# Performance work log

Hardware: AMD Instinct MI355X
Metric: run time of the kernel (lower is better)

The kernel has to match this reference:

```python
import jax, jax.numpy as jnp
import numpy as np

EPS = 1e-12  # F.normalize default eps (denominator = max(norm, eps))


def setup_inputs() -> dict:
    key = jax.random.key(0)
    ks = jax.random.split(key, 8)
    B, FIN, H, W = 4, 256, 64, 64
    N_MEM, SQ = 64, 16           # sqrt_fin = fin**0.5
    POS_CH = 2                    # PosEncoding concatenates one coord channel per dim
    CIN = FIN + POS_CH
    QK = N_MEM * SQ               # 1024
    # PosEncoding buffer: normalized coordinate grid in [-1, 1], shape [2, H, W]
    ys = jnp.linspace(-1.0, 1.0, H, dtype=jnp.float32)
    xs = jnp.linspace(-1.0, 1.0, W, dtype=jnp.float32)
    gy, gx = jnp.meshgrid(ys, xs, indexing='ij')
    pos = jnp.stack([gy, gx], axis=0)
    s = 0.02
    return {
        'x':    jax.random.normal(ks[0], (B, FIN, H, W), jnp.float32),
        'pos':  pos,
        'wq':   jax.random.normal(ks[1], (QK, CIN), jnp.float32) * s,
        'bq':   jnp.zeros((QK,), jnp.float32),
        'wk':   jax.random.normal(ks[2], (QK, CIN), jnp.float32) * s,
        'bk':   jnp.zeros((QK,), jnp.float32),
        'v':    jax.random.normal(ks[3], (N_MEM, FIN), jnp.float32) * s,
        'wout': jax.random.normal(ks[4], (FIN, FIN), jnp.float32) * s,
        'bout': jnp.zeros((FIN,), jnp.float32),
    }


def reference(x, pos, wq, bq, wk, bk, v, wout, bout):
    B, C, H, W = x.shape
    S = H * W
    n_mem, fin = v.shape
    sq = wq.shape[0] // n_mem
    # PosEncoding: concat coordinate channels
    posb = jnp.broadcast_to(pos[None], (B,) + pos.shape)
    xp = jnp.concatenate([x, posb], axis=1).reshape(B, C + pos.shape[0], S)
    # 1x1 conv projections (channel GEMMs)
    q = jnp.einsum('oc,bcs->bos', wq, xp) + bq[None, :, None]  # [B, n_mem*sq, S]
    k = jnp.einsum('oc,bcs->bos', wk, xp) + bk[None, :, None]
    q = q.reshape(B, n_mem, sq, S).transpose(0, 3, 1, 2)  # [B,S,m,sq]
    k = k.reshape(B, n_mem, sq, S).transpose(0, 3, 2, 1)  # [B,S,sq,m]
    # F.normalize: q over last dim (sqrt_fin), k over dim=1 (sqrt_fin)
    qn = q / jnp.maximum(jnp.linalg.norm(q, axis=-1, keepdims=True), EPS)
    kn = k / jnp.maximum(jnp.linalg.norm(k, axis=2, keepdims=True), EPS)
    # attn[b,s,m,n] = qn . kn ; dropout is identity in eval mode.
    # mean over memory slots m commutes with (attn @ v), so fuse:
    attn_mean = jnp.einsum('bsk,bskn->bsn', qn.mean(axis=2), kn)  # [B,S,n_mem]
    mem = attn_mean @ v                                            # [B,S,fin]
    mem = mem.transpose(0, 2, 1).reshape(B, fin, H, W)
    out = jnp.einsum('of,bfhw->bohw', wout, mem) + bout[None, :, None, None]
    return x + out
```

## Files before the change

### kernel.cpp

```cpp
#include <hip/hip_runtime.h>
#include <stdint.h>

#define EPSN 1e-12f

typedef float f32x16 __attribute__((ext_vector_type(16)));
typedef float f32x4 __attribute__((ext_vector_type(4)));
typedef __bf16 bf16x8 __attribute__((ext_vector_type(8)));

__device__ __forceinline__ unsigned short f2bf(float f) {
  union { float f; unsigned int u; } v; v.f = f;
  unsigned int u = v.u + 0x7FFFu + ((v.u >> 16) & 1u);
  return (unsigned short)(u >> 16);
}

#define WQF_OFF 0
#define WKF_OFF (32 * 18 * 64 * 8)
#define WVP_OFF (2 * 32 * 18 * 64 * 8)

__global__ __launch_bounds__(256) void prep_kernel(
    const float* __restrict__ wq, const float* __restrict__ bq,
    const float* __restrict__ wk, const float* __restrict__ bk,
    const float* __restrict__ v, const float* __restrict__ wout,
    unsigned short* __restrict__ wsp) {
  int bid = blockIdx.x;
  if (bid < 512) {
    int isK = bid >= 256;
    int ob = (bid & 255) * 4;
    const float* w = isK ? wk : wq;
    const float* bb = isK ? bk : bq;
    unsigned short* dst = wsp + (isK ? WKF_OFF : WQF_OFF);
    for (int i = threadIdx.x; i < 4 * 129; i += 256) {
      int r = i / 129, q = i - r * 129;
      int o = ob + r, k = q * 2;
      float2 w2 = *(const float2*)(w + o * 258 + k);
      int g = o >> 5, col = o & 31;
      int ks = k >> 4, hi = (k >> 3) & 1, j = k & 7;
      uint32_t pk = (uint32_t)f2bf(w2.x) | ((uint32_t)f2bf(w2.y) << 16);
      *(uint32_t*)(dst + (((g * 18 + ks) * 64 + hi * 32 + col) << 3) + j) = pk;
    }
    for (int i = threadIdx.x; i < 4 * 30; i += 256) {
      int r = i / 30, kk = 258 + (i - r * 30);
      int o = ob + r;
      int g = o >> 5, col = o & 31;
      int ks = kk >> 4, hi = (kk >> 3) & 1, j = kk & 7;
      dst[(((g * 18 + ks) * 64 + hi * 32 + col) << 3) + j] =
          (kk == 258) ? f2bf(bb[o]) : (unsigned short)0;
    }
  } else {
    int idx = (bid - 512) * 256 + threadIdx.x;
    int fc = idx & 15, m = (idx >> 4) & 63, o = idx >> 10;
    const f32x4* wo = (const f32x4*)(wout + o * 256 + fc * 16);
    const f32x4* vm = (const f32x4*)(v + m * 256 + fc * 16);
    float s = 0.f;
#pragma unroll
    for (int f = 0; f < 4; ++f) {
      f32x4 a = wo[f], bvv = vm[f];
      s += a[0]*bvv[0] + a[1]*bvv[1] + a[2]*bvv[2] + a[3]*bvv[3];
    }
    s += __shfl_xor(s, 1, 64);
    s += __shfl_xor(s, 2, 64);
    s += __shfl_xor(s, 4, 64);
    s += __shfl_xor(s, 8, 64);
    if (fc == 0) wsp[WVP_OFF + o * 64 + m] = f2bf(s);
  }
}

#define QSS 33
#define AT 72

__global__ __launch_bounds__(1024, 4) void fused_kernel(
    const float* __restrict__ x, const float* __restrict__ pos,
    const unsigned short* __restrict__ wsp, const float* __restrict__ bout,
    float* __restrict__ out) {
  __shared__ __align__(16) unsigned short xpF[18 * 2 * 32 * 8];
  __shared__ __align__(16) float qbarL[16 * QSS];
  __shared__ __align__(16) unsigned short attnM[32 * AT];
  __shared__ float boutL[256];

  const int tid = threadIdx.x;
  const int lane = tid & 63;
  const int wid = __builtin_amdgcn_readfirstlane(tid >> 6);
  const int px = lane & 31, q2 = lane >> 5;
  const int P0 = blockIdx.x * 32;
  const int b = P0 >> 12, s0 = P0 & 4095;

  uint32_t* xp32 = (uint32_t*)xpF;
  for (int i = tid; i < 32 * 144; i += 1024) {
    int p = i & 31, dcol = i >> 5;
    int c0 = dcol * 2;
    float v0, v1;
    if (c0 < 256) {
      v0 = x[(b * 256 + c0) * 4096 + s0 + p];
      v1 = x[(b * 256 + c0 + 1) * 4096 + s0 + p];
    } else if (c0 == 256) {
      v0 = pos[s0 + p];
      v1 = pos[4096 + s0 + p];
    } else {
      v0 = (c0 == 258) ? 1.0f : 0.0f;
      v1 = 0.0f;
    }
    xp32[(dcol >> 2) * 128 + p * 4 + (dcol & 3)] =
        (uint32_t)f2bf(v0) | ((uint32_t)f2bf(v1) << 16);
  }
  if (tid < 256) boutL[tid] = bout[tid];
  if (tid < 16 * QSS) qbarL[tid] = 0.f;
  __syncthreads();

  const unsigned short* aq = wsp + WQF_OFF + (2 * wid) * 18 * 512 + lane * 8;
  const unsigned short* ak = wsp + WKF_OFF + (2 * wid) * 18 * 512 + lane * 8;

  f32x16 accq0 = (f32x16)0.f, accq1 = (f32x16)0.f,
         acck0 = (f32x16)0.f, acck1 = (f32x16)0.f;
#pragma unroll 3
  for (int ks = 0; ks < 18; ++ks) {
    bf16x8 bv = *(const bf16x8*)&xpF[(ks * 2 + q2) * 256 + px * 8];
    bf16x8 aq0 = *(const bf16x8*)(aq + ks * 512);
    bf16x8 aq1 = *(const bf16x8*)(aq + 9216 + ks * 512);
    bf16x8 ak0 = *(const bf16x8*)(ak + ks * 512);
    bf16x8 ak1 = *(const bf16x8*)(ak + 9216 + ks * 512);
    accq0 = __builtin_amdgcn_mfma_f32_32x32x16_bf16(aq0, bv, accq0, 0, 0, 0);
    accq1 = __builtin_amdgcn_mfma_f32_32x32x16_bf16(aq1, bv, accq1, 0, 0, 0);
    acck0 = __builtin_amdgcn_mfma_f32_32x32x16_bf16(ak0, bv, acck0, 0, 0, 0);
    acck1 = __builtin_amdgcn_mfma_f32_32x32x16_bf16(ak1, bv, acck1, 0, 0, 0);
  }

  {
    float qsum[8];
#pragma unroll
    for (int r = 0; r < 8; ++r) qsum[r] = 0.f;
#pragma unroll
    for (int t = 0; t < 2; ++t) {
      const f32x16 a = t ? accq1 : accq0;
      float s20 = 0.f, s21 = 0.f;
#pragma unroll
      for (int r = 0; r < 8; ++r) {
        s20 = fmaf(a[r], a[r], s20);
        s21 = fmaf(a[r + 8], a[r + 8], s21);
      }
      s20 += __shfl_xor(s20, 32, 64);
      s21 += __shfl_xor(s21, 32, 64);
      float i0 = 1.0f / fmaxf(sqrtf(s20), EPSN);
      float i1 = 1.0f / fmaxf(sqrtf(s21), EPSN);
#pragma unroll
      for (int r = 0; r < 8; ++r) qsum[r] += a[r] * i0 + a[r + 8] * i1;
    }
#pragma unroll
    for (int r = 0; r < 8; ++r) {
      int j = (r & 3) + ((r >> 2) << 3) + (q2 << 2);
      atomicAdd(&qbarL[j * QSS + px], qsum[r] * (1.0f / 64.0f));
    }
  }
  __syncthreads();

  {
    float qb[8];
#pragma unroll
    for (int r = 0; r < 8; ++r) {
      int j = (r & 3) + ((r >> 2) << 3) + (q2 << 2);
      qb[r] = qbarL[j * QSS + px];
    }
#pragma unroll
    for (int t = 0; t < 2; ++t) {
      const f32x16 a = t ? acck1 : acck0;
      float s20 = 0.f, s21 = 0.f, sp0 = 0.f, sp1 = 0.f;
#pragma unroll
      for (int r = 0; r < 8; ++r) {
        s20 = fmaf(a[r], a[r], s20);         sp0 = fmaf(qb[r], a[r], sp0);
        s21 = fmaf(a[r + 8], a[r + 8], s21); sp1 = fmaf(qb[r], a[r + 8], sp1);
      }
      s20 += __shfl_xor(s20, 32, 64);
      s21 += __shfl_xor(s21, 32, 64);
      sp0 += __shfl_xor(sp0, 32, 64);
      sp1 += __shfl_xor(sp1, 32, 64);
      if (q2 == 0) {
        int m0 = wid * 4 + t * 2;
        attnM[px * AT + m0]     = f2bf(sp0 / fmaxf(sqrtf(s20), EPSN));
        attnM[px * AT + m0 + 1] = f2bf(sp1 / fmaxf(sqrtf(s21), EPSN));
      }
    }
  }
  __syncthreads();

  if (wid < 8) {
    f32x16 e = (f32x16)0.f;
    const unsigned short* wv = wsp + WVP_OFF + (wid * 32 + px) * 64 + q2 * 8;
    const unsigned short* ab = &attnM[px * AT + q2 * 8];
#pragma unroll
    for (int ks = 0; ks < 4; ++ks) {
      bf16x8 av = *(const bf16x8*)(wv + ks * 16);
      bf16x8 bv = *(const bf16x8*)(ab + ks * 16);
      e = __builtin_amdgcn_mfma_f32_32x32x16_bf16(av, bv, e, 0, 0, 0);
    }
#pragma unroll
    for (int r = 0; r < 16; ++r) {
      const int o = wid * 32 + (r & 3) + (((r >> 2) & 1) << 3) + (q2 << 2) + ((r >> 3) << 4);
      const int gi = (b * 256 + o) * 4096 + s0 + px;
      out[gi] = x[gi] + boutL[o] + e[r];
    }
  }
}

extern "C" void kernel_launch(void* const* d_in, const int* in_sizes, int n_in,
                              void* d_out, int out_size, void* d_ws, size_t ws_size,
                              hipStream_t stream) {
  const float* x    = (const float*)d_in[0];
  const float* pos  = (const float*)d_in[1];
  const float* wq   = (const float*)d_in[2];
  const float* bq   = (const float*)d_in[3];
  const float* wk   = (const float*)d_in[4];
  const float* bk   = (const float*)d_in[5];
  const float* v    = (const float*)d_in[6];
  const float* wout = (const float*)d_in[7];
  const float* bout = (const float*)d_in[8];
  float* out = (float*)d_out;
  unsigned short* wsp = (unsigned short*)d_ws;

  hipLaunchKernelGGL(prep_kernel, dim3(1536), dim3(256), 0, stream,
                     wq, bq, wk, bk, v, wout, wsp);
  hipLaunchKernelGGL(fused_kernel, dim3(512), dim3(1024), 0, stream,
                     x, pos, wsp, bout, out);
}
```

Measured before the change: 140.9 us.

## Split fused kernel into Q-projection, K-attention and epilogue kernels with wider pixel tiles

Replaces the single fused kernel with three kernels. The first projects Q and reduces the normalized mean into a global qbar buffer using atomics. The second projects K and writes bf16 attention weights to global memory. The third applies the folded V·Wout GEMM with the residual. Each projection block now covers 128 pixels and a quarter of the output channels, so weight tiles are reused across more pixels and each block needs fewer accumulator registers. The cost is staging x twice, global atomics and intermediate round trips, and extra launches.

```diff
diff --git a/kernel.cpp b/kernel.cpp
--- a/kernel.cpp
+++ b/kernel.cpp
@@ -14,8 +14,10 @@
 }
 
 #define WQF_OFF 0
-#define WKF_OFF (32 * 18 * 64 * 8)
-#define WVP_OFF (2 * 32 * 18 * 64 * 8)
+#define WKF_OFF 294912
+#define WVP_OFF 589824
+#define QBG_OFF 606208
+#define ATN_OFF 1130496
 
 __global__ __launch_bounds__(256) void prep_kernel(
     const float* __restrict__ wq, const float* __restrict__ bq,
@@ -46,7 +48,7 @@
       dst[(((g * 18 + ks) * 64 + hi * 32 + col) << 3) + j] =
           (kk == 258) ? f2bf(bb[o]) : (unsigned short)0;
     }
-  } else {
+  } else if (bid < 1536) {
     int idx = (bid - 512) * 256 + threadIdx.x;
     int fc = idx & 15, m = (idx >> 4) & 63, o = idx >> 10;
     const f32x4* wo = (const f32x4*)(wout + o * 256 + fc * 16);
@@ -62,31 +64,19 @@
     s += __shfl_xor(s, 4, 64);
     s += __shfl_xor(s, 8, 64);
     if (fc == 0) wsp[WVP_OFF + o * 64 + m] = f2bf(s);
-  }
-}
-
-#define QSS 33
-#define AT 72
-
-__global__ __launch_bounds__(1024, 4) void fused_kernel(
-    const float* __restrict__ x, const float* __restrict__ pos,
-    const unsigned short* __restrict__ wsp, const float* __restrict__ bout,
-    float* __restrict__ out) {
-  __shared__ __align__(16) unsigned short xpF[18 * 2 * 32 * 8];
-  __shared__ __align__(16) float qbarL[16 * QSS];
-  __shared__ __align__(16) unsigned short attnM[32 * AT];
-  __shared__ float boutL[256];
-
-  const int tid = threadIdx.x;
-  const int lane = tid & 63;
-  const int wid = __builtin_amdgcn_readfirstlane(tid >> 6);
-  const int px = lane & 31, q2 = lane >> 5;
-  const int P0 = blockIdx.x * 32;
-  const int b = P0 >> 12, s0 = P0 & 4095;
-
+  } else {
+    int idx = (bid - 1536) * 256 + threadIdx.x;
+    ((f32x4*)(wsp + QBG_OFF))[idx] = (f32x4)0.f;
+  }
+}
+
+__device__ __forceinline__ void stage128(const float* __restrict__ x,
+                                         const float* __restrict__ pos,
+                                         unsigned short* xpF,
+                                         int b, int s0, int tid) {
   uint32_t* xp32 = (uint32_t*)xpF;
-  for (int i = tid; i < 32 * 144; i += 1024) {
-    int p = i & 31, dcol = i >> 5;
+  for (int i = tid; i < 128 * 144; i += 1024) {
+    int p = i & 127, dcol = i >> 7;
     int c0 = dcol * 2;
     float v0, v1;
     if (c0 < 256) {
@@ -99,104 +89,165 @@
       v0 = (c0 == 258) ? 1.0f : 0.0f;
       v1 = 0.0f;
     }
-    xp32[(dcol >> 2) * 128 + p * 4 + (dcol & 3)] =
+    xp32[(dcol >> 2) * 512 + p * 4 + (dcol & 3)] =
         (uint32_t)f2bf(v0) | ((uint32_t)f2bf(v1) << 16);
   }
+}
+
+__global__ __launch_bounds__(1024, 4) void qproj_kernel(
+    const float* __restrict__ x, const float* __restrict__ pos,
+    const unsigned short* __restrict__ wsp, float* __restrict__ qbarG) {
+  __shared__ __align__(16) unsigned short xpF[18 * 2 * 128 * 8];
+  __shared__ float qbp[16 * 128];
+
+  const int tid = threadIdx.x;
+  const int lane = tid & 63;
+  const int wid = __builtin_amdgcn_readfirstlane(tid >> 6);
+  const int px = lane & 31, q2 = lane >> 5;
+  const int pg = blockIdx.x & 127, og = blockIdx.x >> 7;
+  const int PX0 = pg * 128;
+  const int b = PX0 >> 12, s0 = PX0 & 4095;
+
+  stage128(x, pos, xpF, b, s0, tid);
+  for (int i = tid; i < 16 * 128; i += 1024) qbp[i] = 0.f;
+  __syncthreads();
+
+  const int wot = (wid >> 2) * 2, wp = wid & 3;
+  const unsigned short* a0p = wsp + WQF_OFF + ((og * 8 + wot) * 18 * 64 + lane) * 8;
+  const unsigned short* a1p = a0p + 18 * 512;
+  const unsigned short* bvp = &xpF[(q2 * 128 + wp * 32 + px) * 8];
+
+  f32x16 acc0 = (f32x16)0.f, acc1 = (f32x16)0.f;
+#pragma unroll
+  for (int ks = 0; ks < 18; ++ks) {
+    bf16x8 bv = *(const bf16x8*)(bvp + ks * 2048);
+    bf16x8 a0 = *(const bf16x8*)(a0p + ks * 512);
+    bf16x8 a1 = *(const bf16x8*)(a1p + ks * 512);
+    acc0 = __builtin_amdgcn_mfma_f32_32x32x16_bf16(a0, bv, acc0, 0, 0, 0);
+    acc1 = __builtin_amdgcn_mfma_f32_32x32x16_bf16(a1, bv, acc1, 0, 0, 0);
+  }
+
+  float qsum[8];
+#pragma unroll
+  for (int r = 0; r < 8; ++r) qsum[r] = 0.f;
+#pragma unroll
+  for (int t = 0; t < 2; ++t) {
+    const f32x16 a = t ? acc1 : acc0;
+    float s20 = 0.f, s21 = 0.f;
+#pragma unroll
+    for (int r = 0; r < 8; ++r) {
+      s20 = fmaf(a[r], a[r], s20);
+      s21 = fmaf(a[r + 8], a[r + 8], s21);
+    }
+    s20 += __shfl_xor(s20, 32, 64);
+    s21 += __shfl_xor(s21, 32, 64);
+    float i0 = 1.0f / fmaxf(sqrtf(s20), EPSN);
+    float i1 = 1.0f / fmaxf(sqrtf(s21), EPSN);
+#pragma unroll
+    for (int r = 0; r < 8; ++r) qsum[r] += a[r] * i0 + a[r + 8] * i1;
+  }
+#pragma unroll
+  for (int r = 0; r < 8; ++r) {
+    int j = (r & 3) + ((r >> 2) << 3) + (q2 << 2);
+    atomicAdd(&qbp[j * 128 + wp * 32 + px], qsum[r] * (1.0f / 64.0f));
+  }
+  __syncthreads();
+  for (int i = tid; i < 2048; i += 1024) {
+    int j = i >> 7, p = i & 127;
+    atomicAdd(qbarG + (PX0 + p) * 16 + j, qbp[i]);
+  }
+}
+
+__global__ __launch_bounds__(1024, 4) void kattn_kernel(
+    const float* __restrict__ x, const float* __restrict__ pos,
+    const unsigned short* __restrict__ wsp, const float* __restrict__ qbarG,
+    unsigned short* __restrict__ attnG) {
+  __shared__ __align__(16) unsigned short xpF[18 * 2 * 128 * 8];
+
+  const int tid = threadIdx.x;
+  const int lane = tid & 63;
+  const int wid = __builtin_amdgcn_readfirstlane(tid >> 6);
+  const int px = lane & 31, q2 = lane >> 5;
+  const int pg = blockIdx.x & 127, og = blockIdx.x >> 7;
+  const int PX0 = pg * 128;
+  const int b = PX0 >> 12, s0 = PX0 & 4095;
+
+  stage128(x, pos, xpF, b, s0, tid);
+  __syncthreads();
+
+  const int wot = (wid >> 2) * 2, wp = wid & 3;
+  const unsigned short* a0p = wsp + WKF_OFF + ((og * 8 + wot) * 18 * 64 + lane) * 8;
+  const unsigned short* a1p = a0p + 18 * 512;
+  const unsigned short* bvp = &xpF[(q2 * 128 + wp * 32 + px) * 8];
+
+  f32x16 acc0 = (f32x16)0.f, acc1 = (f32x16)0.f;
+#pragma unroll
+  for (int ks = 0; ks < 18; ++ks) {
+    bf16x8 bv = *(const bf16x8*)(bvp + ks * 2048);
+    bf16x8 a0 = *(const bf16x8*)(a0p + ks * 512);
+    bf16x8 a1 = *(const bf16x8*)(a1p + ks * 512);
+    acc0 = __builtin_amdgcn_mfma_f32_32x32x16_bf16(a0, bv, acc0, 0, 0, 0);
+    acc1 = __builtin_amdgcn_mfma_f32_32x32x16_bf16(a1, bv, acc1, 0, 0, 0);
+  }
+
+  const int pxg = PX0 + wp * 32 + px;
+  float qb[8];
+#pragma unroll
+  for (int r = 0; r < 8; ++r) {
+    int j = (r & 3) + ((r >> 2) << 3) + (q2 << 2);
+    qb[r] = qbarG[pxg * 16 + j];
+  }
+#pragma unroll
+  for (int t = 0; t < 2; ++t) {
+    const f32x16 a = t ? acc1 : acc0;
+    float s20 = 0.f, s21 = 0.f, sp0 = 0.f, sp1 = 0.f;
+#pragma unroll
+    for (int r = 0; r < 8; ++r) {
+      s20 = fmaf(a[r], a[r], s20);         sp0 = fmaf(qb[r], a[r], sp0);
+      s21 = fmaf(a[r + 8], a[r + 8], s21); sp1 = fmaf(qb[r], a[r + 8], sp1);
+    }
+    s20 += __shfl_xor(s20, 32, 64);
+    s21 += __shfl_xor(s21, 32, 64);
+    sp0 += __shfl_xor(sp0, 32, 64);
+    sp1 += __shfl_xor(sp1, 32, 64);
+    if (q2 == 0) {
+      int m0 = og * 16 + (wot + t) * 2;
+      attnG[pxg * 64 + m0]     = f2bf(sp0 / fmaxf(sqrtf(s20), EPSN));
+      attnG[pxg * 64 + m0 + 1] = f2bf(sp1 / fmaxf(sqrtf(s21), EPSN));
+    }
+  }
+}
+
+__global__ __launch_bounds__(1024, 8) void epi_kernel(
+    const float* __restrict__ x, const unsigned short* __restrict__ wsp,
+    const unsigned short* __restrict__ attnG, const float* __restrict__ bout,
+    float* __restrict__ out) {
+  __shared__ float boutL[256];
+  const int tid = threadIdx.x;
+  const int lane = tid & 63;
+  const int wid = __builtin_amdgcn_readfirstlane(tid >> 6);
+  const int px = lane & 31, q2 = lane >> 5;
+  const int P0 = blockIdx.x * 64;
+  const int b = P0 >> 12, s0 = P0 & 4095;
+
   if (tid < 256) boutL[tid] = bout[tid];
-  if (tid < 16 * QSS) qbarL[tid] = 0.f;
-  __syncthreads();
-
-  const unsigned short* aq = wsp + WQF_OFF + (2 * wid) * 18 * 512 + lane * 8;
-  const unsigned short* ak = wsp + WKF_OFF + (2 * wid) * 18 * 512 + lane * 8;
-
-  f32x16 accq0 = (f32x16)0.f, accq1 = (f32x16)0.f,
-         acck0 = (f32x16)0.f, acck1 = (f32x16)0.f;
-#pragma unroll 3
-  for (int ks = 0; ks < 18; ++ks) {
-    bf16x8 bv = *(const bf16x8*)&xpF[(ks * 2 + q2) * 256 + px * 8];
-    bf16x8 aq0 = *(const bf16x8*)(aq + ks * 512);
-    bf16x8 aq1 = *(const bf16x8*)(aq + 9216 + ks * 512);
-    bf16x8 ak0 = *(const bf16x8*)(ak + ks * 512);
-    bf16x8 ak1 = *(const bf16x8*)(ak + 9216 + ks * 512);
-    accq0 = __builtin_amdgcn_mfma_f32_32x32x16_bf16(aq0, bv, accq0, 0, 0, 0);
-    accq1 = __builtin_amdgcn_mfma_f32_32x32x16_bf16(aq1, bv, accq1, 0, 0, 0);
-    acck0 = __builtin_amdgcn_mfma_f32_32x32x16_bf16(ak0, bv, acck0, 0, 0, 0);
-    acck1 = __builtin_amdgcn_mfma_f32_32x32x16_bf16(ak1, bv, acck1, 0, 0, 0);
-  }
-
-  {
-    float qsum[8];
-#pragma unroll
-    for (int r = 0; r < 8; ++r) qsum[r] = 0.f;
-#pragma unroll
-    for (int t = 0; t < 2; ++t) {
-      const f32x16 a = t ? accq1 : accq0;
-      float s20 = 0.f, s21 = 0.f;
-#pragma unroll
-      for (int r = 0; r < 8; ++r) {
-        s20 = fmaf(a[r], a[r], s20);
-        s21 = fmaf(a[r + 8], a[r + 8], s21);
-      }
-      s20 += __shfl_xor(s20, 32, 64);
-      s21 += __shfl_xor(s21, 32, 64);
-      float i0 = 1.0f / fmaxf(sqrtf(s20), EPSN);
-      float i1 = 1.0f / fmaxf(sqrtf(s21), EPSN);
-#pragma unroll
-      for (int r = 0; r < 8; ++r) qsum[r] += a[r] * i0 + a[r + 8] * i1;
-    }
-#pragma unroll
-    for (int r = 0; r < 8; ++r) {
-      int j = (r & 3) + ((r >> 2) << 3) + (q2 << 2);
-      atomicAdd(&qbarL[j * QSS + px], qsum[r] * (1.0f / 64.0f));
-    }
-  }
-  __syncthreads();
-
-  {
-    float qb[8];
-#pragma unroll
-    for (int r = 0; r < 8; ++r) {
-      int j = (r & 3) + ((r >> 2) << 3) + (q2 << 2);
-      qb[r] = qbarL[j * QSS + px];
-    }
-#pragma unroll
-    for (int t = 0; t < 2; ++t) {
-      const f32x16 a = t ? acck1 : acck0;
-      float s20 = 0.f, s21 = 0.f, sp0 = 0.f, sp1 = 0.f;
-#pragma unroll
-      for (int r = 0; r < 8; ++r) {
-        s20 = fmaf(a[r], a[r], s20);         sp0 = fmaf(qb[r], a[r], sp0);
-        s21 = fmaf(a[r + 8], a[r + 8], s21); sp1 = fmaf(qb[r], a[r + 8], sp1);
-      }
-      s20 += __shfl_xor(s20, 32, 64);
-      s21 += __shfl_xor(s21, 32, 64);
-      sp0 += __shfl_xor(sp0, 32, 64);
-      sp1 += __shfl_xor(sp1, 32, 64);
-      if (q2 == 0) {
-        int m0 = wid * 4 + t * 2;
-        attnM[px * AT + m0]     = f2bf(sp0 / fmaxf(sqrtf(s20), EPSN));
-        attnM[px * AT + m0 + 1] = f2bf(sp1 / fmaxf(sqrtf(s21), EPSN));
-      }
-    }
-  }
-  __syncthreads();
-
-  if (wid < 8) {
-    f32x16 e = (f32x16)0.f;
-    const unsigned short* wv = wsp + WVP_OFF + (wid * 32 + px) * 64 + q2 * 8;
-    const unsigned short* ab = &attnM[px * AT + q2 * 8];
-#pragma unroll
-    for (int ks = 0; ks < 4; ++ks) {
-      bf16x8 av = *(const bf16x8*)(wv + ks * 16);
-      bf16x8 bv = *(const bf16x8*)(ab + ks * 16);
-      e = __builtin_amdgcn_mfma_f32_32x32x16_bf16(av, bv, e, 0, 0, 0);
-    }
-#pragma unroll
-    for (int r = 0; r < 16; ++r) {
-      const int o = wid * 32 + (r & 3) + (((r >> 2) & 1) << 3) + (q2 << 2) + ((r >> 3) << 4);
-      const int gi = (b * 256 + o) * 4096 + s0 + px;
-      out[gi] = x[gi] + boutL[o] + e[r];
-    }
+  __syncthreads();
+
+  const int otile = wid >> 1, pxt = wid & 1;
+  f32x16 e = (f32x16)0.f;
+  const unsigned short* wv = wsp + WVP_OFF + (otile * 32 + px) * 64 + q2 * 8;
+  const unsigned short* ab = attnG + (P0 + pxt * 32 + px) * 64 + q2 * 8;
+#pragma unroll
+  for (int ks = 0; ks < 4; ++ks) {
+    bf16x8 av = *(const bf16x8*)(wv + ks * 16);
+    bf16x8 bv = *(const bf16x8*)(ab + ks * 16);
+    e = __builtin_amdgcn_mfma_f32_32x32x16_bf16(av, bv, e, 0, 0, 0);
+  }
+#pragma unroll
+  for (int r = 0; r < 16; ++r) {
+    const int o = otile * 32 + (r & 3) + (((r >> 2) & 1) << 3) + (q2 << 2) + ((r >> 3) << 4);
+    const int gi = (b * 256 + o) * 4096 + s0 + pxt * 32 + px;
+    out[gi] = x[gi] + boutL[o] + e[r];
   }
 }
 
@@ -214,9 +265,15 @@
   const float* bout = (const float*)d_in[8];
   float* out = (float*)d_out;
   unsigned short* wsp = (unsigned short*)d_ws;
-
-  hipLaunchKernelGGL(prep_kernel, dim3(1536), dim3(256), 0, stream,
+  float* qbarG = (float*)(wsp + QBG_OFF);
+  unsigned short* attnG = wsp + ATN_OFF;
+
+  hipLaunchKernelGGL(prep_kernel, dim3(1792), dim3(256), 0, stream,
                      wq, bq, wk, bk, v, wout, wsp);
-  hipLaunchKernelGGL(fused_kernel, dim3(512), dim3(1024), 0, stream,
-                     x, pos, wsp, bout, out);
-}
+  hipLaunchKernelGGL(qproj_kernel, dim3(512), dim3(1024), 0, stream,
+                     x, pos, wsp, qbarG);
+  hipLaunchKernelGGL(kattn_kernel, dim3(512), dim3(1024), 0, stream,
+                     x, pos, wsp, qbarG, attnG);
+  hipLaunchKernelGGL(epi_kernel, dim3(256), dim3(1024), 0, stream,
+                     x, wsp, attnG, bout, out);
+}
```

After: 199.1 us. +41.3%, slower.
